# Optimization experiments

Hardware: AMD Instinct MI355X
Metric: run time of the kernel (lower is better)

## Reference

```python
import jax, jax.numpy as jnp
import numpy as np

H = 12  # num_heads (init_kwargs)


def setup_inputs() -> dict:
    key = jax.random.key(0)
    ks = jax.random.split(key, 8)
    B, N, W = 32, 576, 16      # batch, num patches, local window
    d, P = 768, 4              # d_model, num_prompts
    s = lambda k, shape: jax.random.normal(k, shape, jnp.float32) * 0.02
    return dict(
        x=jax.random.normal(ks[0], (B, N, 1536), jnp.float32),
        y=jax.random.normal(ks[1], (B, N * W, 1024), jnp.float32),
        Wx=s(ks[2], (d, 1536)), bx=jnp.zeros((d,), jnp.float32),
        Wy=s(ks[3], (d, 1024)), by=jnp.zeros((d,), jnp.float32),
        prompt=jax.random.normal(ks[4], (1, P, d), jnp.float32),
        in_proj_w=s(ks[5], (3 * d, d)), in_proj_b=jnp.zeros((3 * d,), jnp.float32),
        out_w=s(ks[6], (d, d)), out_b=jnp.zeros((d,), jnp.float32),
    )


def reference(x, y, Wx, bx, Wy, by, prompt, in_proj_w, in_proj_b, out_w, out_b):
    B, N, _ = x.shape
    d = Wx.shape[0]
    W = y.shape[1] // N          # local kv window = 16
    P = prompt.shape[1]          # num prompts
    Dh = d // H
    scale = 1.0 / float(np.sqrt(Dh))

    x_proj = x @ Wx.T + bx                      # [B,N,d]
    y_proj = (y @ Wy.T + by).reshape(B, N, W, d)  # [B,N,W,d] local kv windows

    # queries per patch i: [x_proj[:, i], prompts] -> [B,N,1+P,d]
    pr = jnp.broadcast_to(prompt[:, None], (B, N, P, d))
    q_in = jnp.concatenate([x_proj[:, :, None, :], pr], axis=2)

    Wq, Wk, Wv = jnp.split(in_proj_w, 3, axis=0)
    bq, bk, bv = jnp.split(in_proj_b, 3)
    q = (q_in @ Wq.T + bq).reshape(B, N, 1 + P, H, Dh)
    k = (y_proj @ Wk.T + bk).reshape(B, N, W, H, Dh)
    v = (y_proj @ Wv.T + bv).reshape(B, N, W, H, Dh)

    scores = jnp.einsum('bnqhd,bnkhd->bnhqk', q, k) * scale  # [B,N,H,1+P,W]
    attn = jax.nn.softmax(scores, axis=-1)
    o = jnp.einsum('bnhqk,bnkhd->bnqhd', attn, v).reshape(B, N, 1 + P, d)
    out = o @ out_w.T + out_b                   # [B,N,1+P,d]
    return out.reshape(B, N * (1 + P), d)
```

## Files before the change

### kernel.cpp

```cpp
#include <hip/hip_runtime.h>
#include <hip/hip_bf16.h>


typedef __attribute__((ext_vector_type(8))) short bf16x8;
typedef __attribute__((ext_vector_type(4))) float f32x4;
typedef __attribute__((ext_vector_type(2))) float f32x2;
typedef __attribute__((ext_vector_type(8))) unsigned short u16x8;

__device__ __forceinline__ float bf2f(unsigned short u) {
  union { unsigned int i; float f; } x; x.i = ((unsigned int)u) << 16; return x.f;
}
__device__ __forceinline__ unsigned short f2b(float f) {
  union { float f; unsigned int i; } x; x.f = f;
  unsigned int u = x.i;
  return (unsigned short)((u + 0x7fffu + ((u >> 16) & 1u)) >> 16);
}
__device__ __forceinline__ unsigned int cvtpk(float lo, float hi) {
  unsigned int r;
  asm("v_cvt_pk_bf16_f32 %0, %1, %2" : "=v"(r) : "v"(lo), "v"(hi));
  return r;
}
__device__ __forceinline__ f32x2 bf2x(unsigned int u) {
  union { unsigned int i; float f; } lo, hi;
  lo.i = u << 16; hi.i = u & 0xFFFF0000u;
  f32x2 r; r[0] = lo.f; r[1] = hi.f; return r;
}
__device__ __forceinline__ void pkfma(f32x2& acc, f32x2 a, f32x2 b) {
  asm("v_pk_fma_f32 %0, %1, %2, %0" : "+v"(acc) : "v"(a), "v"(b));
}

#define GLDS(gaddr, laddr) \
  __builtin_amdgcn_global_load_lds( \
      (const __attribute__((address_space(1))) unsigned int*)(gaddr), \
      (__attribute__((address_space(3))) unsigned int*)(laddr), 16, 0, 0)

__global__ void k_cvt(const float* __restrict__ src, unsigned short* __restrict__ dst, long n8) {
  long stride = (long)gridDim.x * blockDim.x;
  for (long i = (long)blockIdx.x * blockDim.x + threadIdx.x; i < n8; i += stride) {
    float4 a = ((const float4*)src)[2 * i];
    float4 b = ((const float4*)src)[2 * i + 1];
    u16x8 t = { f2b(a.x), f2b(a.y), f2b(a.z), f2b(a.w),
                f2b(b.x), f2b(b.y), f2b(b.z), f2b(b.w) };
    ((u16x8*)dst)[i] = t;
  }
}

__global__ __launch_bounds__(256) void k_tr(const float* __restrict__ src,
                                            unsigned short* __restrict__ dst,
                                            int R, int C) {
  __shared__ float t[32][33];
  int bx = blockIdx.x * 32, by = blockIdx.y * 32;
  int lx = threadIdx.x & 31, ly = threadIdx.x >> 5;
#pragma unroll
  for (int s = 0; s < 32; s += 8)
    t[ly + s][lx] = src[(long)(by + ly + s) * C + bx + lx];
  __syncthreads();
#pragma unroll
  for (int s = 0; s < 32; s += 8)
    dst[(long)(bx + ly + s) * R + by + lx] = f2b(t[lx][ly + s]);
}

__global__ void k_zf(float* __restrict__ p, int n) {
  int i = blockIdx.x * 256 + threadIdx.x;
  if (i < n) p[i] = 0.f;
}

__global__ void k_bfuse(const float* __restrict__ ipw, const float* __restrict__ ipb,
                        const float* __restrict__ bx, const float* __restrict__ by,
                        float* __restrict__ bqx, float* __restrict__ bkv) {
  int o    = blockIdx.x * 4 + (threadIdx.x >> 6);
  int lane = threadIdx.x & 63;
  int sec  = o / 768, jj = o - sec * 768;
  const float* Arow = ipw + (long)o * 768;
  const float* vb   = (sec == 0) ? bx : by;
  float s = 0.f;
  for (int k = lane; k < 768; k += 64) s += Arow[k] * vb[k];
#pragma unroll
  for (int d = 32; d > 0; d >>= 1) s += __shfl_down(s, d);
  if (lane == 0) {
    s += ipb[o];
    if (sec == 0) bqx[jj] = s;
    else if (sec == 1) bkv[jj] = s;
    else bkv[768 + jj] = s;
  }
}

__global__ void k_qprompt(const float* __restrict__ ipw, const float* __restrict__ ipb,
                          const float* __restrict__ prompt, unsigned short* __restrict__ qpf) {
  int o    = blockIdx.x * 4 + (threadIdx.x >> 6);
  int lane = threadIdx.x & 63;
  int p = o / 768, j = o - p * 768;
  const float* Wqr = ipw + (long)j * 768;
  const float* pr  = prompt + (long)p * 768;
  float s = 0.f;
  for (int k = lane; k < 768; k += 64) s += Wqr[k] * pr[k];
#pragma unroll
  for (int d = 32; d > 0; d >>= 1) s += __shfl_down(s, d);
  if (lane == 0) qpf[o] = f2b(s + ipb[j]);
}

template <typename OutT>
__global__ __launch_bounds__(256) void k_gemm(const unsigned short* __restrict__ A,
                                              const unsigned short* __restrict__ Bw,
                                              const float* __restrict__ bias,
                                              OutT* __restrict__ C,
                                              int M, int Nn, int K, int nbx) {
  const int tid  = threadIdx.x;
  const int lane = tid & 63, wid = tid >> 6;
  const int wm = wid >> 1, wn = wid & 1;
  const int lr = lane & 15, lk = lane >> 4;

  const int nwg = gridDim.x, orig = blockIdx.x;
  const int q8 = nwg >> 3, r8 = nwg & 7, xc = orig & 7;
  const int wg = (xc < r8 ? xc * (q8 + 1) : r8 * (q8 + 1) + (xc - r8) * q8) + (orig >> 3);
  const int bn = wg % nbx, bm = wg / nbx;
  const int m0 = bm * 128, n0 = bn * 128;

  __shared__ __attribute__((aligned(16))) unsigned short As[2][128 * 32];
  __shared__ __attribute__((aligned(16))) unsigned short Bs[2][128 * 32];

  f32x4 acc[4][4];
#pragma unroll
  for (int nt = 0; nt < 4; ++nt) {
    float bv = bias[n0 + wn * 64 + nt * 16 + lr];
    f32x4 bvv = {bv, bv, bv, bv};
#pragma unroll
    for (int mt = 0; mt < 4; ++mt) acc[mt][nt] = bvv;
  }

  const int NS = K >> 5;
  const int crow = lane >> 2, ck8 = (lane & 3) * 8;

  auto stage = [&](int buf, int ks) {
#pragma unroll
    for (int i = 0; i < 2; ++i) {
      int c = wid * 2 + i;
      int row = c * 16 + crow;
      GLDS(&A[(long)(m0 + row) * K + ks * 32 + ck8], &As[buf][c * 512]);
      GLDS(&Bw[(long)(n0 + row) * K + ks * 32 + ck8], &Bs[buf][c * 512]);
    }
  };

  stage(0, 0);
  __syncthreads();

  for (int t = 0; t < NS; ++t) {
    const int cur = t & 1, nb = cur ^ 1;
    if (t + 1 < NS) stage(nb, t + 1);
    bf16x8 af[4], bfr[4];
#pragma unroll
    for (int mt = 0; mt < 4; ++mt)
      af[mt] = *(const bf16x8*)&As[cur][(wm * 64 + mt * 16 + lr) * 32 + lk * 8];
#pragma unroll
    for (int nt = 0; nt < 4; ++nt)
      bfr[nt] = *(const bf16x8*)&Bs[cur][(wn * 64 + nt * 16 + lr) * 32 + lk * 8];
#pragma unroll
    for (int mt = 0; mt < 4; ++mt)
#pragma unroll
      for (int nt = 0; nt < 4; ++nt)
        acc[mt][nt] = __builtin_amdgcn_mfma_f32_16x16x32_bf16(af[mt], bfr[nt], acc[mt][nt], 0, 0, 0);
    __syncthreads();
  }

#pragma unroll
  for (int mt = 0; mt < 4; ++mt)
#pragma unroll
    for (int nt = 0; nt < 4; ++nt) {
      int col = n0 + wn * 64 + nt * 16 + lr;
#pragma unroll
      for (int r = 0; r < 4; ++r) {
        int row = m0 + wm * 64 + mt * 16 + lk * 4 + r;
        float v = acc[mt][nt][r];
        if constexpr (sizeof(OutT) == 4) C[(long)row * Nn + col] = v;
        else                             C[(long)row * Nn + col] = f2b(v);
      }
    }
}

template <typename OutT>
__global__ __launch_bounds__(512, 2) void k_gemm8(const unsigned short* __restrict__ A,
                                                  const unsigned short* __restrict__ Bw,
                                                  const float* __restrict__ bias,
                                                  OutT* __restrict__ C,
                                                  int M, int Nn, int K, int nbx) {
  const int tid  = threadIdx.x;
  const int lane = tid & 63, wid = tid >> 6;
  const int wm = wid >> 2, wn = wid & 3;
  const int lr = lane & 15, lk = lane >> 4;

  const int nwg = gridDim.x, orig = blockIdx.x;
  const int q8 = nwg >> 3, r8 = nwg & 7, xc = orig & 7;
  const int wg = (xc < r8 ? xc * (q8 + 1) : r8 * (q8 + 1) + (xc - r8) * q8) + (orig >> 3);
  const int bn = wg % nbx, bm = wg / nbx;
  const long m0 = (long)bm * 256, n0 = (long)bn * 256;

  __shared__ __attribute__((aligned(16))) unsigned short As[2][2][8192];
  __shared__ __attribute__((aligned(16))) unsigned short Bs[2][2][8192];

  f32x4 acc[8][4];
#pragma unroll
  for (int nt = 0; nt < 4; ++nt) {
    float bv = bias[n0 + wn * 64 + nt * 16 + lr];
    f32x4 bvv = {bv, bv, bv, bv};
#pragma unroll
    for (int mt = 0; mt < 8; ++mt) acc[mt][nt] = bvv;
  }

  const int NT = K >> 6;

  auto stage = [&](int buf, int kt, int isB, int h) {
#pragma unroll
    for (int j = 0; j < 2; ++j) {
      int c   = j * 8 + wid;
      int row = c * 8 + (lane >> 3);
      int col = ((lane & 7) * 8) ^ ((row & 7) << 3);
      const unsigned short* g = isB
          ? &Bw[(n0 + h * 128 + row) * (long)K + kt * 64 + col]
          : &A [(m0 + h * 128 + row) * (long)K + kt * 64 + col];
      unsigned short* l = isB ? &Bs[buf][h][c * 512] : &As[buf][h][c * 512];
      GLDS(g, l);
    }
  };
  auto ldsA = [&](int buf, int mt, int kk) -> bf16x8 {
    int r = mt * 16 + lr;
    int off = r * 128 + ((kk * 64 + lk * 16) ^ ((lr & 7) << 4));
    return *(const bf16x8*)((const char*)&As[buf][wm][0] + off);
  };
  auto ldsB = [&](int buf, int nt, int kk) -> bf16x8 {
    int r = (wn & 1) * 64 + nt * 16 + lr;
    int off = r * 128 + ((kk * 64 + lk * 16) ^ ((lr & 7) << 4));
    return *(const bf16x8*)((const char*)&Bs[buf][wn >> 1][0] + off);
  };

  stage(0, 0, 0, 0); stage(0, 0, 0, 1); stage(0, 0, 1, 0); stage(0, 0, 1, 1);
  if (NT > 1) {
    stage(1, 1, 0, 0);
    asm volatile("s_waitcnt vmcnt(2)" ::: "memory");
  } else {
    asm volatile("s_waitcnt vmcnt(0)" ::: "memory");
  }
  __builtin_amdgcn_s_barrier();

  for (int u = 0; u < NT; ++u) {
    const int cb = u & 1;
    bf16x8 a[4][2], b0[2][2], b1[2][2];

#pragma unroll
    for (int mt = 0; mt < 4; ++mt) { a[mt][0] = ldsA(cb, mt, 0); a[mt][1] = ldsA(cb, mt, 1); }
#pragma unroll
    for (int nt = 0; nt < 2; ++nt) { b0[nt][0] = ldsB(cb, nt, 0); b0[nt][1] = ldsB(cb, nt, 1); }
    if (u + 1 < NT) stage(cb ^ 1, u + 1, 0, 1);
    __builtin_amdgcn_s_barrier();
    asm volatile("s_waitcnt lgkmcnt(0)" ::: "memory");
    __builtin_amdgcn_s_setprio(1);
#pragma unroll
    for (int mt = 0; mt < 4; ++mt)
#pragma unroll
      for (int nt = 0; nt < 2; ++nt)
#pragma unroll
        for (int kk = 0; kk < 2; ++kk)
          acc[mt][nt] = __builtin_amdgcn_mfma_f32_16x16x32_bf16(a[mt][kk], b0[nt][kk], acc[mt][nt], 0, 0, 0);
    __builtin_amdgcn_s_setprio(0);
    __builtin_amdgcn_s_barrier();

#pragma unroll
    for (int nt = 0; nt < 2; ++nt) { b1[nt][0] = ldsB(cb, 2 + nt, 0); b1[nt][1] = ldsB(cb, 2 + nt, 1); }
    if (u + 1 < NT) stage(cb ^ 1, u + 1, 1, 0);
    __builtin_amdgcn_s_barrier();
    asm volatile("s_waitcnt lgkmcnt(0)" ::: "memory");
    __builtin_amdgcn_s_setprio(1);
#pragma unroll
    for (int mt = 0; mt < 4; ++mt)
#pragma unroll
      for (int nt = 0; nt < 2; ++nt)
#pragma unroll
        for (int kk = 0; kk < 2; ++kk)
          acc[mt][2 + nt] = __builtin_amdgcn_mfma_f32_16x16x32_bf16(a[mt][kk], b1[nt][kk], acc[mt][2 + nt], 0, 0, 0);
    __builtin_amdgcn_s_setprio(0);
    __builtin_amdgcn_s_barrier();

#pragma unroll
    for (int mt = 0; mt < 4; ++mt) { a[mt][0] = ldsA(cb, 4 + mt, 0); a[mt][1] = ldsA(cb, 4 + mt, 1); }
    if (u + 1 < NT) stage(cb ^ 1, u + 1, 1, 1);
    __builtin_amdgcn_s_barrier();
    asm volatile("s_waitcnt lgkmcnt(0)" ::: "memory");
    __builtin_amdgcn_s_setprio(1);
#pragma unroll
    for (int mt = 0; mt < 4; ++mt)
#pragma unroll
      for (int nt = 0; nt < 2; ++nt)
#pragma unroll
        for (int kk = 0; kk < 2; ++kk)
          acc[4 + mt][2 + nt] = __builtin_amdgcn_mfma_f32_16x16x32_bf16(a[mt][kk], b1[nt][kk], acc[4 + mt][2 + nt], 0, 0, 0);
    __builtin_amdgcn_s_setprio(0);
    __builtin_amdgcn_s_barrier();

    if (u + 2 < NT) stage(cb, u + 2, 0, 0);
    __builtin_amdgcn_s_barrier();
    __builtin_amdgcn_s_setprio(1);
#pragma unroll
    for (int mt = 0; mt < 4; ++mt)
#pragma unroll
      for (int nt = 0; nt < 2; ++nt)
#pragma unroll
        for (int kk = 0; kk < 2; ++kk)
          acc[4 + mt][nt] = __builtin_amdgcn_mfma_f32_16x16x32_bf16(a[mt][kk], b0[nt][kk], acc[4 + mt][nt], 0, 0, 0);
    __builtin_amdgcn_s_setprio(0);
    if (u + 2 < NT)       asm volatile("s_waitcnt vmcnt(2)" ::: "memory");
    else if (u + 1 < NT)  asm volatile("s_waitcnt vmcnt(0)" ::: "memory");
    __builtin_amdgcn_s_barrier();
  }

#pragma unroll
  for (int mt = 0; mt < 8; ++mt)
#pragma unroll
    for (int nt = 0; nt < 4; ++nt) {
      long col = n0 + wn * 64 + nt * 16 + lr;
#pragma unroll
      for (int r = 0; r < 4; ++r) {
        long row = m0 + wm * 128 + mt * 16 + lk * 4 + r;
        float v = acc[mt][nt][r];
        if constexpr (sizeof(OutT) == 4) C[row * Nn + col] = v;
        else                             C[row * Nn + col] = f2b(v);
      }
    }
}

__global__ __launch_bounds__(256) void k_attn(const unsigned short* __restrict__ kv,
                                              const unsigned short* __restrict__ qx,
                                              const unsigned short* __restrict__ qp,
                                              unsigned short* __restrict__ o) {
  __shared__ __attribute__((aligned(16))) unsigned short Ks[16 * 776];
  __shared__ __attribute__((aligned(16))) unsigned short Qs[5 * 768];
  __shared__ float Ss[60 * 16];
  const int tid = threadIdx.x;
  const long pp = (long)blockIdx.x;

  for (int i = tid; i < 16 * 96; i += 256) {
    int r = i / 96, c8 = i - r * 96;
    *(u16x8*)&Ks[r * 776 + c8 * 8] =
        *(const u16x8*)&kv[(pp * 16 + r) * 1536 + c8 * 8];
  }
  for (int i = tid; i < 5 * 96; i += 256) {
    int r = i / 96, c8 = i - r * 96;
    const unsigned short* src = (r == 0) ? &qx[pp * 768 + c8 * 8]
                                         : &qp[(long)(r - 1) * 768 + c8 * 8];
    *(u16x8*)&Qs[r * 768 + c8 * 8] = *(const u16x8*)src;
  }
  __syncthreads();

  for (int idx = tid; idx < 960; idx += 256) {
    int w = idx & 15, rest = idx >> 4;
    int h = rest % 12, q5 = rest / 12;
    const unsigned int* kr = (const unsigned int*)&Ks[w * 776 + h * 64];
    const unsigned int* qr = (const unsigned int*)&Qs[q5 * 768 + h * 64];
    f32x2 a2 = {0.f, 0.f};
#pragma unroll
    for (int j = 0; j < 8; ++j) {
      uint4 kw = *(const uint4*)(kr + j * 4);
      uint4 qw = *(const uint4*)(qr + j * 4);
      pkfma(a2, bf2x(kw.x), bf2x(qw.x));
      pkfma(a2, bf2x(kw.y), bf2x(qw.y));
      pkfma(a2, bf2x(kw.z), bf2x(qw.z));
      pkfma(a2, bf2x(kw.w), bf2x(qw.w));
    }
    float s = (a2[0] + a2[1]) * 0.125f;
    float m = s;
#pragma unroll
    for (int d = 1; d < 16; d <<= 1) m = fmaxf(m, __shfl_xor(m, d));
    float e = __expf(s - m);
    float sum = e;
#pragma unroll
    for (int d = 1; d < 16; d <<= 1) sum += __shfl_xor(sum, d);
    Ss[rest * 16 + w] = e / sum;
  }
  __syncthreads();

  for (int idx = tid; idx < 480; idx += 256) {
    int d8 = idx % 96, q5 = idx / 96;
    int h = d8 >> 3;
    const float* arow = &Ss[(q5 * 12 + h) * 16];
    const unsigned short* vbase = &kv[pp * 16 * 1536 + 768 + d8 * 8];
    f32x2 a0 = {0.f, 0.f}, a1 = {0.f, 0.f}, a2v = {0.f, 0.f}, a3 = {0.f, 0.f};
#pragma unroll
    for (int w = 0; w < 16; ++w) {
      uint4 vv = *(const uint4*)&vbase[(long)w * 1536];
      float aw = arow[w];
      f32x2 aw2 = {aw, aw};
      pkfma(a0,  bf2x(vv.x), aw2);
      pkfma(a1,  bf2x(vv.y), aw2);
      pkfma(a2v, bf2x(vv.z), aw2);
      pkfma(a3,  bf2x(vv.w), aw2);
    }
    uint4 pk;
    pk.x = cvtpk(a0[0],  a0[1]);
    pk.y = cvtpk(a1[0],  a1[1]);
    pk.z = cvtpk(a2v[0], a2v[1]);
    pk.w = cvtpk(a3[0],  a3[1]);
    *(uint4*)&o[(pp * 5 + q5) * 768 + d8 * 8] = pk;
  }
}

extern "C" void kernel_launch(void* const* d_in, const int* in_sizes, int n_in,
                              void* d_out, int out_size, void* d_ws, size_t ws_size,
                              hipStream_t stream) {
  const float* x      = (const float*)d_in[0];
  const float* y      = (const float*)d_in[1];
  const float* Wx     = (const float*)d_in[2];
  const float* bx     = (const float*)d_in[3];
  const float* Wy     = (const float*)d_in[4];
  const float* by     = (const float*)d_in[5];
  const float* prompt = (const float*)d_in[6];
  const float* ipw    = (const float*)d_in[7];
  const float* ipb    = (const float*)d_in[8];
  const float* outw   = (const float*)d_in[9];
  const float* outb   = (const float*)d_in[10];
  float* out = (float*)d_out;

  char* ws = (char*)d_ws;
  size_t off = 0;
  auto alloc = [&](size_t bytes) -> void* {
    void* p = ws + off; off += (bytes + 255) & ~(size_t)255; return p;
  };
  unsigned short* kvb  = (unsigned short*)alloc(294912UL * 1536 * 2);
  unsigned short* qxb  = (unsigned short*)alloc(18432UL * 768 * 2);
  unsigned short* ob   = (unsigned short*)alloc(92160UL * 768 * 2);
  unsigned short* Wqx  = (unsigned short*)alloc(768UL * 1536 * 2);
  unsigned short* Wkv  = (unsigned short*)alloc(1536UL * 1024 * 2);
  unsigned short* oww  = (unsigned short*)alloc(768UL * 768 * 2);
  unsigned short* qpf  = (unsigned short*)alloc(4UL * 768 * 2);
  float*          bqx  = (float*)alloc(768 * 4);
  float*          bkv  = (float*)alloc(1536 * 4);
  unsigned short* ipwb = (unsigned short*)alloc(2304UL * 768 * 2);
  unsigned short* WxT  = (unsigned short*)alloc(1536UL * 768 * 2);
  unsigned short* WyT  = (unsigned short*)alloc(1024UL * 768 * 2);
  float*          zb   = (float*)alloc(1536 * 4);
  unsigned short* xb   = ob;
  unsigned short* ybc  = (unsigned short*)(ws + off);
  long rpc = (long)((ws_size - off) / (1024 * 2)) & ~255L;
  if (rpc > 294912) rpc = 294912;
  if (rpc < 256) rpc = 256;

  k_cvt<<<dim3(288), dim3(256), 0, stream>>>(outw, oww, 768L * 768 / 8);
  k_cvt<<<dim3(864), dim3(256), 0, stream>>>(ipw, ipwb, 2304L * 768 / 8);
  k_tr<<<dim3(48, 24), dim3(256), 0, stream>>>(Wx, WxT, 768, 1536);
  k_tr<<<dim3(32, 24), dim3(256), 0, stream>>>(Wy, WyT, 768, 1024);
  k_zf<<<dim3(6), dim3(256), 0, stream>>>(zb, 1536);
  k_gemm<unsigned short><<<dim3(6 * 12), dim3(256), 0, stream>>>(
      ipwb, WxT, zb, Wqx, 768, 1536, 768, 12);
  k_gemm<unsigned short><<<dim3(6 * 8), dim3(256), 0, stream>>>(
      ipwb + 768 * 768, WyT, zb, Wkv, 768, 1024, 768, 8);
  k_gemm<unsigned short><<<dim3(6 * 8), dim3(256), 0, stream>>>(
      ipwb + 1536 * 768, WyT, zb, Wkv + 768 * 1024, 768, 1024, 768, 8);
  k_bfuse<<<dim3(576), dim3(256), 0, stream>>>(ipw, ipb, bx, by, bqx, bkv);
  k_qprompt<<<dim3(768), dim3(256), 0, stream>>>(ipw, ipb, prompt, qpf);

  k_cvt<<<dim3(2048), dim3(256), 0, stream>>>(x, xb, 18432L * 1536 / 8);
  k_gemm<unsigned short><<<dim3(144 * 6), dim3(256), 0, stream>>>(
      xb, Wqx, bqx, qxb, 18432, 768, 1536, 6);

  long row0 = 0;
  while (row0 < 294912) {
    long mc = 294912 - row0 < rpc ? 294912 - row0 : rpc;
    k_cvt<<<dim3(2048), dim3(256), 0, stream>>>(y + row0 * 1024, ybc, mc * 128);
    k_gemm8<unsigned short><<<dim3((int)(mc / 256) * 6), dim3(512), 0, stream>>>(
        ybc, Wkv, bkv, kvb + row0 * 1536, (int)mc, 1536, 1024, 6);
    row0 += mc;
  }

  k_attn<<<dim3(18432), dim3(256), 0, stream>>>(kvb, qxb, qpf, ob);

  k_gemm8<float><<<dim3(360 * 3), dim3(512), 0, stream>>>(
      ob, oww, outb, out, 92160, 768, 768, 3);
}
```

Baseline: 2.141 ms.

## Store K in head-major layout from GEMM epilogue and drop LDS K staging in attention

The KV projection GEMM epilogue now writes K in a per-patch head-major layout ([h][w][64]) and V as a compact [w][768] block, so each attention thread can read its K row directly from global memory. The attention kernel drops the shared-memory K staging. Each of 192 threads computes all 5 query scores for one (head, window) pair, reusing its K registers across queries, and occupancy is hinted at 6 blocks. The cost is scattered 2-byte stores in the GEMM epilogue and idle threads during the score phase.

```diff
diff --git a/kernel.cpp b/kernel.cpp
--- a/kernel.cpp
+++ b/kernel.cpp
@@ -177,7 +177,7 @@
     }
 }
 
-template <typename OutT>
+template <bool KVL, typename OutT>
 __global__ __launch_bounds__(512, 2) void k_gemm8(const unsigned short* __restrict__ A,
                                                   const unsigned short* __restrict__ Bw,
                                                   const float* __restrict__ bias,
@@ -320,27 +320,30 @@
       for (int r = 0; r < 4; ++r) {
         long row = m0 + wm * 128 + mt * 16 + lk * 4 + r;
         float v = acc[mt][nt][r];
-        if constexpr (sizeof(OutT) == 4) C[row * Nn + col] = v;
-        else                             C[row * Nn + col] = f2b(v);
+        if constexpr (KVL) {
+          long pp = row >> 4; int w = (int)(row & 15);
+          long addr;
+          if (col < 768) addr = pp * 24576 + (col >> 6) * 1024 + w * 64 + (col & 63);
+          else           addr = pp * 24576 + 12288 + (long)w * 768 + (col - 768);
+          C[addr] = f2b(v);
+        } else if constexpr (sizeof(OutT) == 4) {
+          C[row * Nn + col] = v;
+        } else {
+          C[row * Nn + col] = f2b(v);
+        }
       }
     }
 }
 
-__global__ __launch_bounds__(256) void k_attn(const unsigned short* __restrict__ kv,
-                                              const unsigned short* __restrict__ qx,
-                                              const unsigned short* __restrict__ qp,
-                                              unsigned short* __restrict__ o) {
-  __shared__ __attribute__((aligned(16))) unsigned short Ks[16 * 776];
+__global__ __launch_bounds__(256, 6) void k_attn(const unsigned short* __restrict__ kv,
+                                                 const unsigned short* __restrict__ qx,
+                                                 const unsigned short* __restrict__ qp,
+                                                 unsigned short* __restrict__ o) {
   __shared__ __attribute__((aligned(16))) unsigned short Qs[5 * 768];
   __shared__ float Ss[60 * 16];
   const int tid = threadIdx.x;
   const long pp = (long)blockIdx.x;
 
-  for (int i = tid; i < 16 * 96; i += 256) {
-    int r = i / 96, c8 = i - r * 96;
-    *(u16x8*)&Ks[r * 776 + c8 * 8] =
-        *(const u16x8*)&kv[(pp * 16 + r) * 1536 + c8 * 8];
-  }
   for (int i = tid; i < 5 * 96; i += 256) {
     int r = i / 96, c8 = i - r * 96;
     const unsigned short* src = (r == 0) ? &qx[pp * 768 + c8 * 8]
@@ -349,30 +352,42 @@
   }
   __syncthreads();
 
-  for (int idx = tid; idx < 960; idx += 256) {
-    int w = idx & 15, rest = idx >> 4;
-    int h = rest % 12, q5 = rest / 12;
-    const unsigned int* kr = (const unsigned int*)&Ks[w * 776 + h * 64];
-    const unsigned int* qr = (const unsigned int*)&Qs[q5 * 768 + h * 64];
-    f32x2 a2 = {0.f, 0.f};
-#pragma unroll
-    for (int j = 0; j < 8; ++j) {
-      uint4 kw = *(const uint4*)(kr + j * 4);
-      uint4 qw = *(const uint4*)(qr + j * 4);
-      pkfma(a2, bf2x(kw.x), bf2x(qw.x));
-      pkfma(a2, bf2x(kw.y), bf2x(qw.y));
-      pkfma(a2, bf2x(kw.z), bf2x(qw.z));
-      pkfma(a2, bf2x(kw.w), bf2x(qw.w));
-    }
-    float s = (a2[0] + a2[1]) * 0.125f;
-    float m = s;
-#pragma unroll
-    for (int d = 1; d < 16; d <<= 1) m = fmaxf(m, __shfl_xor(m, d));
-    float e = __expf(s - m);
-    float sum = e;
-#pragma unroll
-    for (int d = 1; d < 16; d <<= 1) sum += __shfl_xor(sum, d);
-    Ss[rest * 16 + w] = e / sum;
+  if (tid < 192) {
+    const int h = tid >> 4, w = tid & 15;
+    const uint4* kr = (const uint4*)&kv[pp * 24576 + h * 1024 + w * 64];
+    f32x2 s2[5];
+#pragma unroll
+    for (int q5 = 0; q5 < 5; ++q5) { s2[q5][0] = 0.f; s2[q5][1] = 0.f; }
+#pragma unroll
+    for (int half = 0; half < 2; ++half) {
+      uint4 kk0 = kr[half * 4 + 0], kk1 = kr[half * 4 + 1],
+            kk2 = kr[half * 4 + 2], kk3 = kr[half * 4 + 3];
+#pragma unroll
+      for (int q5 = 0; q5 < 5; ++q5) {
+        const uint4* qr = (const uint4*)&Qs[q5 * 768 + h * 64 + half * 32];
+#pragma unroll
+        for (int j = 0; j < 4; ++j) {
+          uint4 kkj = (j == 0) ? kk0 : (j == 1) ? kk1 : (j == 2) ? kk2 : kk3;
+          uint4 qw = qr[j];
+          pkfma(s2[q5], bf2x(kkj.x), bf2x(qw.x));
+          pkfma(s2[q5], bf2x(kkj.y), bf2x(qw.y));
+          pkfma(s2[q5], bf2x(kkj.z), bf2x(qw.z));
+          pkfma(s2[q5], bf2x(kkj.w), bf2x(qw.w));
+        }
+      }
+    }
+#pragma unroll
+    for (int q5 = 0; q5 < 5; ++q5) {
+      float s = (s2[q5][0] + s2[q5][1]) * 0.125f;
+      float m = s;
+#pragma unroll
+      for (int d = 1; d < 16; d <<= 1) m = fmaxf(m, __shfl_xor(m, d));
+      float e = __expf(s - m);
+      float sum = e;
+#pragma unroll
+      for (int d = 1; d < 16; d <<= 1) sum += __shfl_xor(sum, d);
+      Ss[(q5 * 12 + h) * 16 + w] = e / sum;
+    }
   }
   __syncthreads();
 
@@ -380,11 +395,11 @@
     int d8 = idx % 96, q5 = idx / 96;
     int h = d8 >> 3;
     const float* arow = &Ss[(q5 * 12 + h) * 16];
-    const unsigned short* vbase = &kv[pp * 16 * 1536 + 768 + d8 * 8];
+    const unsigned short* vbase = &kv[pp * 24576 + 12288 + d8 * 8];
     f32x2 a0 = {0.f, 0.f}, a1 = {0.f, 0.f}, a2v = {0.f, 0.f}, a3 = {0.f, 0.f};
 #pragma unroll
     for (int w = 0; w < 16; ++w) {
-      uint4 vv = *(const uint4*)&vbase[(long)w * 1536];
+      uint4 vv = *(const uint4*)&vbase[(long)w * 768];
       float aw = arow[w];
       f32x2 aw2 = {aw, aw};
       pkfma(a0,  bf2x(vv.x), aw2);
@@ -463,13 +478,13 @@
   while (row0 < 294912) {
     long mc = 294912 - row0 < rpc ? 294912 - row0 : rpc;
     k_cvt<<<dim3(2048), dim3(256), 0, stream>>>(y + row0 * 1024, ybc, mc * 128);
-    k_gemm8<unsigned short><<<dim3((int)(mc / 256) * 6), dim3(512), 0, stream>>>(
+    k_gemm8<true, unsigned short><<<dim3((int)(mc / 256) * 6), dim3(512), 0, stream>>>(
         ybc, Wkv, bkv, kvb + row0 * 1536, (int)mc, 1536, 1024, 6);
     row0 += mc;
   }
 
   k_attn<<<dim3(18432), dim3(256), 0, stream>>>(kvb, qxb, qpf, ob);
 
-  k_gemm8<float><<<dim3(360 * 3), dim3(512), 0, stream>>>(
+  k_gemm8<false, float><<<dim3(360 * 3), dim3(512), 0, stream>>>(
       ob, oww, outb, out, 92160, 768, 768, 3);
 }
```

Measured after the change: 2.101 ms. About the same (-1.9%).
